# Optimization experiments

Hardware: AMD Instinct MI355X
Metric: run time of the kernel (lower is better)

Reference implementation:

```python
import jax, jax.numpy as jnp
import numpy as np

EPS = 1e-5

def _ln(x, w, b):
    m = jnp.mean(x, axis=-1, keepdims=True)
    var = jnp.mean((x - m) ** 2, axis=-1, keepdims=True)
    return (x - m) / jnp.sqrt(var + EPS) * w + b

def setup_inputs() -> dict:
    key = jax.random.key(0)
    ks = jax.random.split(key, 24)
    B, Hh, Ww, C = 8, 96, 96, 512
    L = Hh * Ww
    heads, Ck, Cv, hidden = 8, 512, 512, 2048
    s = 0.02
    d = {
        'x': jax.random.normal(ks[0], (B, L, C), jnp.float32),
        'v': jax.random.normal(ks[1], (B, L, C), jnp.float32),
        'H': Hh, 'W': Ww,
        'ln1_w': jnp.ones((C,), jnp.float32), 'ln1_b': jnp.zeros((C,), jnp.float32),
        'lnv_w': jnp.ones((C,), jnp.float32), 'lnv_b': jnp.zeros((C,), jnp.float32),
        'ln2_w': jnp.ones((C,), jnp.float32), 'ln2_b': jnp.zeros((C,), jnp.float32),
        'wq': jax.random.normal(ks[2], (Ck, C), jnp.float32) * s,
        'bq': jnp.zeros((Ck,), jnp.float32),
        'wk': jax.random.normal(ks[3], (Ck, C), jnp.float32) * s,
        'bk': jnp.zeros((Ck,), jnp.float32),
        'wv': jax.random.normal(ks[4], (Cv, C), jnp.float32) * s,
        'bv': jnp.zeros((Cv,), jnp.float32),
        'wr': jax.random.normal(ks[5], (C, Cv), jnp.float32) * s,
        'br': jnp.zeros((C,), jnp.float32),
        'fc1_w': jax.random.normal(ks[6], (hidden, C), jnp.float32) * s,
        'fc1_b': jnp.zeros((hidden,), jnp.float32),
        'fc2_w': jax.random.normal(ks[7], (C, hidden), jnp.float32) * s,
        'fc2_b': jnp.zeros((C,), jnp.float32),
    }
    return d

def reference(x, v, H, W, ln1_w, ln1_b, lnv_w, lnv_b, ln2_w, ln2_b,
              wq, bq, wk, bk, wv, bv, wr, br, fc1_w, fc1_b, fc2_w, fc2_b):
    B, L, C = x.shape
    heads = 8
    Ck, Cv = wq.shape[0], wv.shape[0]
    dk, dv = Ck // heads, Cv // heads

    shortcut = x
    xn = _ln(x, ln1_w, ln1_b)             # (B,L,C)
    vn = _ln(v, lnv_w, lnv_b)             # (B,L,C)

    # 1x1 convs == per-pixel linear over channels
    q = xn @ wq.T + bq                     # (B,L,Ck)
    k = vn @ wk.T + bk                     # (B,L,Ck)
    val = vn @ wv.T + bv                   # (B,L,Cv)

    q = q.reshape(B, L, heads, dk)
    k = k.reshape(B, L, heads, dk)
    val = val.reshape(B, L, heads, dv)

    k_sm = jax.nn.softmax(k, axis=1)       # softmax over spatial dim (torch dim=2 on (n,ck,hw))
    q_sm = jax.nn.softmax(q, axis=3)       # softmax over per-head key channels (torch dim=1)

    # context: (B, heads, dk, dv) = key @ value^T
    context = jnp.einsum('blhk,blhv->bhkv', k_sm, val)
    # attended: (B, heads, dv, L) = context^T @ query  (channel-major like torch)
    attended = jnp.einsum('bhkv,blhk->bhvl', context, q_sm)
    agg = attended.reshape(B, Cv, L)        # concat heads along channels

    reproj = jnp.einsum('oc,bcl->bol', wr, agg) + br[None, :, None]  # (B,C,L)
    x_bcl = jnp.transpose(xn, (0, 2, 1))    # residual inside attention (normed x, channel-major)
    attn_bcl = reproj + x_bcl               # (B,C,L) ~ torch (B,C,H,W) contiguous
    # faithful to torch .view(B, H*W, v_dim): raw row-major reinterpret, no transpose
    attn = attn_bcl.reshape(B, L, C)

    x1 = attn + shortcut
    h = _ln(x1, ln2_w, ln2_b)
    h = jax.nn.gelu(h @ fc1_w.T + fc1_b, approximate=False)
    h = h @ fc2_w.T + fc2_b
    out = x1 + h
    return out
```

## Files before the change

### kernel.cpp

```cpp
#include <hip/hip_runtime.h>
#include <math.h>

typedef unsigned short u16;
typedef unsigned int   u32;
typedef __bf16 bf16x8 __attribute__((ext_vector_type(8)));
typedef float  floatx4 __attribute__((ext_vector_type(4)));

#define DEVFN static __device__ __forceinline__

#define Bb   8
#define Ll   9216
#define Cc   512
#define BL   73728
#define HID  2048

DEVFN float bfu2f(u16 u) { union { u32 i; float f; } z; z.i = ((u32)u) << 16; return z.f; }
DEVFN u16 f2bfu(float f) {
    union { float f; u32 i; } z; z.f = f;
    u32 i = z.i;
    i += 0x7fffu + ((i >> 16) & 1u);
    return (u16)(i >> 16);
}

DEVFN void unpack8(uint4 v, float* x) {
    x[0] = bfu2f(v.x & 0xffff); x[1] = bfu2f(v.x >> 16);
    x[2] = bfu2f(v.y & 0xffff); x[3] = bfu2f(v.y >> 16);
    x[4] = bfu2f(v.z & 0xffff); x[5] = bfu2f(v.z >> 16);
    x[6] = bfu2f(v.w & 0xffff); x[7] = bfu2f(v.w >> 16);
}
DEVFN uint4 pack8(const float* x) {
    uint4 v;
    v.x = (u32)f2bfu(x[0]) | ((u32)f2bfu(x[1]) << 16);
    v.y = (u32)f2bfu(x[2]) | ((u32)f2bfu(x[3]) << 16);
    v.z = (u32)f2bfu(x[4]) | ((u32)f2bfu(x[5]) << 16);
    v.w = (u32)f2bfu(x[6]) | ((u32)f2bfu(x[7]) << 16);
    return v;
}

DEVFN void async16(const void* g, void* l) {
    __builtin_amdgcn_global_load_lds((const __attribute__((address_space(1))) void*)g,
                                     (__attribute__((address_space(3))) void*)l, 16, 0, 0);
}

__global__ __launch_bounds__(256) void f2b(const float* __restrict__ s, u16* __restrict__ d, int n) {
    const int i = blockIdx.x * 256 + threadIdx.x;
    if (i < n) d[i] = f2bfu(s[i]);
}

__global__ __launch_bounds__(256) void ln512(const float* __restrict__ in_,
                                             const float* __restrict__ w, const float* __restrict__ b,
                                             u16* __restrict__ out) {
    const int wave = threadIdx.x >> 6, lane = threadIdx.x & 63;
    const int row = blockIdx.x * 4 + wave;
    float x[8];
    const float4* p = (const float4*)(in_ + (size_t)row * 512);
    float4 a = p[lane * 2], c = p[lane * 2 + 1];
    x[0] = a.x; x[1] = a.y; x[2] = a.z; x[3] = a.w;
    x[4] = c.x; x[5] = c.y; x[6] = c.z; x[7] = c.w;
    float s = 0.f, s2 = 0.f;
    #pragma unroll
    for (int j = 0; j < 8; ++j) { s += x[j]; s2 += x[j] * x[j]; }
    #pragma unroll
    for (int off = 32; off >= 1; off >>= 1) { s += __shfl_xor(s, off); s2 += __shfl_xor(s2, off); }
    const float m   = s * (1.f / 512.f);
    const float var = s2 * (1.f / 512.f) - m * m;
    const float r   = rsqrtf(var + 1e-5f);
    float y[8];
    const int c0 = lane * 8;
    #pragma unroll
    for (int j = 0; j < 8; ++j)
        y[j] = (x[j] - m) * r * w[c0 + j] + b[c0 + j];
    ((uint4*)(out + (size_t)row * 512))[lane] = pack8(y);
}

template<int EPI>
__global__ __launch_bounds__(256) void gemm_bt(
    const u16* __restrict__ A, const u16* __restrict__ W, const float* __restrict__ bias,
    const float* __restrict__ resid, void* __restrict__ out_,
    int M, int N, int K, int wbatch) {
    __shared__ __align__(16) u16 sA[128 * 32];
    __shared__ __align__(16) u16 sB[128 * 32];
    const int t = threadIdx.x;
    const int wv = t >> 6, lane = t & 63;
    const int row0 = blockIdx.y * 128, col0 = blockIdx.x * 128;
    const u16* Wb = W + (wbatch > 0 ? (size_t)(row0 / wbatch) * (size_t)N * (size_t)K : 0);
    const int wr = wv >> 1, wc = wv & 1;
    floatx4 acc[4][4] = {};
    const int rr = t >> 2, kc = t & 3;
    const int mrow = lane & 15, koff = (lane >> 4) * 8;

    for (int k0 = 0; k0 < K; k0 += 32) {
        #pragma unroll
        for (int i = 0; i < 2; ++i) {
            const u16* ga = A  + (size_t)(row0 + i * 64 + rr) * K + (k0 + kc * 8);
            const u16* gb = Wb + (size_t)(col0 + i * 64 + rr) * K + (k0 + kc * 8);
            async16(ga, (char*)sA + (i * 256 + wv * 64) * 16);
            async16(gb, (char*)sB + (i * 256 + wv * 64) * 16);
        }
        __syncthreads();
        bf16x8 af[4], bq[4];
        #pragma unroll
        for (int mi = 0; mi < 4; ++mi)
            af[mi] = *(const bf16x8*)&sA[(wr * 64 + mi * 16 + mrow) * 32 + koff];
        #pragma unroll
        for (int ni = 0; ni < 4; ++ni)
            bq[ni] = *(const bf16x8*)&sB[(wc * 64 + ni * 16 + mrow) * 32 + koff];
        #pragma unroll
        for (int mi = 0; mi < 4; ++mi)
            #pragma unroll
            for (int ni = 0; ni < 4; ++ni)
                acc[mi][ni] = __builtin_amdgcn_mfma_f32_16x16x32_bf16(af[mi], bq[ni], acc[mi][ni], 0, 0, 0);
        __syncthreads();
    }
    #pragma unroll
    for (int mi = 0; mi < 4; ++mi) {
        #pragma unroll
        for (int ni = 0; ni < 4; ++ni) {
            const int col = col0 + wc * 64 + ni * 16 + mrow;
            const float bb = bias[col];
            #pragma unroll
            for (int r = 0; r < 4; ++r) {
                const int row = row0 + wr * 64 + mi * 16 + (lane >> 4) * 4 + r;
                float v2 = acc[mi][ni][r] + bb;
                if (EPI == 1) v2 = 0.5f * v2 * (1.f + erff(v2 * 0.70710678118654752f));
                if (EPI == 2) {
                    v2 += resid[(size_t)row * N + col];
                    ((float*)out_)[(size_t)row * N + col] = v2;
                } else {
                    ((u16*)out_)[(size_t)row * N + col] = f2bfu(v2);
                }
            }
        }
    }
}

__global__ __launch_bounds__(256) void kstats1(const u16* __restrict__ k,
                                               float* __restrict__ pmax, float* __restrict__ psum) {
    const int cg = blockIdx.x, lc = blockIdx.y, b = blockIdx.z;
    const int t = threadIdx.x, cl = t & 15, lsub = t >> 4;
    const int c = cg * 16 + cl;
    const u16* base = k + ((size_t)b * Ll + (size_t)lc * 1152) * 512 + c;
    float m = -1e30f, s = 0.f;
    for (int i = 0; i < 72; ++i) {
        const float x = bfu2f(base[(size_t)(lsub + i * 16) * 512]);
        const float nm = fmaxf(m, x);
        s = s * __expf(m - nm) + __expf(x - nm);
        m = nm;
    }
    __shared__ float sm[256], ss[256];
    sm[t] = m; ss[t] = s;
    __syncthreads();
    if (t < 16) {
        float M = sm[t], S = ss[t];
        for (int j = 1; j < 16; ++j) {
            const float m2 = sm[j * 16 + t], s2 = ss[j * 16 + t];
            const float nm = fmaxf(M, m2);
            S = S * __expf(M - nm) + s2 * __expf(m2 - nm);
            M = nm;
        }
        const int cid = b * 512 + cg * 16 + t;
        pmax[(size_t)cid * 8 + lc] = M;
        psum[(size_t)cid * 8 + lc] = S;
    }
}

__global__ __launch_bounds__(256) void kstats2(const float* __restrict__ pmax, const float* __restrict__ psum,
                                               float* __restrict__ kmax, float* __restrict__ ksum) {
    const int id = blockIdx.x * 256 + threadIdx.x;
    float M = -1e30f, S = 0.f;
    for (int lc = 0; lc < 8; ++lc) {
        const float m2 = pmax[(size_t)id * 8 + lc], s2 = psum[(size_t)id * 8 + lc];
        const float nm = fmaxf(M, m2);
        S = S * __expf(M - nm) + s2 * __expf(m2 - nm);
        M = nm;
    }
    kmax[id] = M; ksum[id] = S;
}

__global__ __launch_bounds__(256) void zerof(float* __restrict__ p) {
    p[blockIdx.x * 256 + threadIdx.x] = 0.f;
}

__global__ __launch_bounds__(256) void ctxk(const u16* __restrict__ k, const u16* __restrict__ val,
                                            const float* __restrict__ kmax, float* __restrict__ ctx) {
    const int lc = blockIdx.x, h = blockIdx.y, b = blockIdx.z;
    const int t = threadIdx.x;
    const int li = t >> 6, cc = t & 63;
    const int dkt = t >> 4, dvt = t & 15;
    __shared__ __align__(16) float ke[4][64];
    __shared__ __align__(16) float ve[4][64];
    float acc[4][4] = {};
    const size_t rowbase = ((size_t)b * Ll + (size_t)lc * 1152) * 512 + h * 64;
    const float km = kmax[b * 512 + h * 64 + cc];
    for (int l0 = 0; l0 < 1152; l0 += 4) {
        const float kf = bfu2f(k[rowbase + (size_t)(l0 + li) * 512 + cc]);
        const float vf = bfu2f(val[rowbase + (size_t)(l0 + li) * 512 + cc]);
        __syncthreads();
        ke[li][cc] = __expf(kf - km);
        ve[li][cc] = vf;
        __syncthreads();
        #pragma unroll
        for (int li2 = 0; li2 < 4; ++li2) {
            const float4 kk = *(const float4*)&ke[li2][dkt * 4];
            const float4 vv = *(const float4*)&ve[li2][dvt * 4];
            acc[0][0] += kk.x * vv.x; acc[0][1] += kk.x * vv.y; acc[0][2] += kk.x * vv.z; acc[0][3] += kk.x * vv.w;
            acc[1][0] += kk.y * vv.x; acc[1][1] += kk.y * vv.y; acc[1][2] += kk.y * vv.z; acc[1][3] += kk.y * vv.w;
            acc[2][0] += kk.z * vv.x; acc[2][1] += kk.z * vv.y; acc[2][2] += kk.z * vv.z; acc[2][3] += kk.z * vv.w;
            acc[3][0] += kk.w * vv.x; acc[3][1] += kk.w * vv.y; acc[3][2] += kk.w * vv.z; acc[3][3] += kk.w * vv.w;
        }
    }
    float* cp = ctx + (((size_t)(b * 8 + h) * 64 + dkt * 4) * 64 + dvt * 4);
    #pragma unroll
    for (int i = 0; i < 4; ++i)
        #pragma unroll
        for (int j = 0; j < 4; ++j)
            atomicAdd(&cp[(size_t)i * 64 + j], acc[i][j]);
}

__global__ __launch_bounds__(256) void qsm(u16* __restrict__ q) {
    const size_t seg = (size_t)blockIdx.x * 256 + threadIdx.x;
    u16* p = q + seg * 64;
    float x[64];
    #pragma unroll
    for (int i = 0; i < 8; ++i) { uint4 v = ((const uint4*)p)[i]; unpack8(v, x + i * 8); }
    float m = x[0];
    #pragma unroll
    for (int i = 1; i < 64; ++i) m = fmaxf(m, x[i]);
    float s = 0.f;
    #pragma unroll
    for (int i = 0; i < 64; ++i) { x[i] = __expf(x[i] - m); s += x[i]; }
    const float inv = 1.f / s;
    #pragma unroll
    for (int i = 0; i < 64; ++i) x[i] *= inv;
    #pragma unroll
    for (int i = 0; i < 8; ++i) ((uint4*)p)[i] = pack8(x + i * 8);
}

__global__ __launch_bounds__(256) void weffk(const float* __restrict__ ctx, const float* __restrict__ wr,
                                             const float* __restrict__ ksum, u16* __restrict__ weff) {
    const int b = blockIdx.y;
    const int idx = blockIdx.x * 256 + threadIdx.x;
    const int co = idx >> 9, ck = idx & 511;
    const int h = ck >> 6, dk = ck & 63;
    const float* wrp = wr + (size_t)co * 512 + h * 64;
    const float* cp = ctx + ((size_t)(b * 8 + h) * 64 + dk) * 64;
    float s = 0.f;
    #pragma unroll 8
    for (int dv = 0; dv < 64; ++dv) s += wrp[dv] * cp[dv];
    s /= ksum[b * 512 + ck];
    weff[((size_t)b * 512 + co) * 512 + ck] = f2bfu(s);
}

__global__ __launch_bounds__(256) void assemble(const u16* __restrict__ attnCT, const u16* __restrict__ xn,
                                                const float* __restrict__ x, float* __restrict__ x1) {
    const int ct = blockIdx.x, lt = blockIdx.y, b = blockIdx.z;
    __shared__ float tile[64][65];
    const int t = threadIdx.x, j = t & 63, i0 = t >> 6;
    const size_t base = ((size_t)b * Ll + (size_t)lt * 64) * 512 + ct * 64;
    #pragma unroll
    for (int ii = 0; ii < 16; ++ii) {
        const int i = i0 + ii * 4;
        tile[i][j] = bfu2f(attnCT[base + (size_t)i * 512 + j]) + bfu2f(xn[base + (size_t)i * 512 + j]);
    }
    __syncthreads();
    const size_t bb = (size_t)b * Ll * 512;
    #pragma unroll
    for (int ii = 0; ii < 16; ++ii) {
        const int co = i0 + ii * 4;
        const size_t n = (size_t)(ct * 64 + co) * Ll + (size_t)lt * 64 + j;
        x1[bb + n] = tile[j][co] + x[bb + n];
    }
}

extern "C" void kernel_launch(void* const* d_in, const int* in_sizes, int n_in,
                              void* d_out, int out_size, void* d_ws, size_t ws_size,
                              hipStream_t stream) {
    (void)in_sizes; (void)n_in; (void)out_size; (void)ws_size;
    const float* x    = (const float*)d_in[0];
    const float* v    = (const float*)d_in[1];
    const float* ln1w = (const float*)d_in[4];
    const float* ln1b = (const float*)d_in[5];
    const float* lnvw = (const float*)d_in[6];
    const float* lnvb = (const float*)d_in[7];
    const float* ln2w = (const float*)d_in[8];
    const float* ln2b = (const float*)d_in[9];
    const float* wq   = (const float*)d_in[10]; const float* bq_ = (const float*)d_in[11];
    const float* wk   = (const float*)d_in[12]; const float* bk_ = (const float*)d_in[13];
    const float* wv_  = (const float*)d_in[14]; const float* bv_ = (const float*)d_in[15];
    const float* wr_  = (const float*)d_in[16]; const float* br_ = (const float*)d_in[17];
    const float* f1w  = (const float*)d_in[18]; const float* f1b = (const float*)d_in[19];
    const float* f2w  = (const float*)d_in[20]; const float* f2b_ = (const float*)d_in[21];
    float* out = (float*)d_out;

    char* ws = (char*)d_ws;
    u16*   xn   = (u16*)(ws);
    u16*   vn   = (u16*)(ws + 75497472ull);
    u16*   q    = (u16*)(ws + 150994944ull);
    u16*   kk   = (u16*)(ws + 226492416ull);
    u16*   val  = (u16*)(ws + 301989888ull);
    float* x1   = (float*)(ws + 377487360ull);
    float* kmax = (float*)(ws + 528482304ull);
    float* ksum = (float*)(ws + 528498688ull);
    float* pmax = (float*)(ws + 528515072ull);
    float* psum = (float*)(ws + 528646144ull);
    float* ctx  = (float*)(ws + 528777216ull);
    u16*   weff = (u16*)(ws + 529825792ull);
    u16*   bwq  = (u16*)(ws + 534020096ull);
    u16*   bwk  = (u16*)(ws + 534544384ull);
    u16*   bwv  = (u16*)(ws + 535068672ull);
    u16*   bf1  = (u16*)(ws + 535592960ull);
    u16*   bf2  = (u16*)(ws + 537690112ull);

    f2b<<<1024, 256, 0, stream>>>(wq,  bwq, 262144);
    f2b<<<1024, 256, 0, stream>>>(wk,  bwk, 262144);
    f2b<<<1024, 256, 0, stream>>>(wv_, bwv, 262144);
    f2b<<<4096, 256, 0, stream>>>(f1w, bf1, 1048576);
    f2b<<<4096, 256, 0, stream>>>(f2w, bf2, 1048576);
    ln512<<<18432, 256, 0, stream>>>(x, ln1w, ln1b, xn);
    ln512<<<18432, 256, 0, stream>>>(v, lnvw, lnvb, vn);
    gemm_bt<0><<<dim3(4, 576), 256, 0, stream>>>(xn, bwq, bq_, nullptr, q,   BL, 512, 512, 0);
    gemm_bt<0><<<dim3(4, 576), 256, 0, stream>>>(vn, bwk, bk_, nullptr, kk,  BL, 512, 512, 0);
    gemm_bt<0><<<dim3(4, 576), 256, 0, stream>>>(vn, bwv, bv_, nullptr, val, BL, 512, 512, 0);
    kstats1<<<dim3(32, 8, 8), 256, 0, stream>>>(kk, pmax, psum);
    kstats2<<<16, 256, 0, stream>>>(pmax, psum, kmax, ksum);
    zerof<<<1024, 256, 0, stream>>>(ctx);
    ctxk<<<dim3(8, 8, 8), 256, 0, stream>>>(kk, val, kmax, ctx);
    qsm<<<2304, 256, 0, stream>>>(q);
    weffk<<<dim3(1024, 8), 256, 0, stream>>>(ctx, wr_, ksum, weff);
    gemm_bt<0><<<dim3(4, 576), 256, 0, stream>>>(q, weff, br_, nullptr, vn , BL, 512, 512, Ll);
    assemble<<<dim3(8, 144, 8), 256, 0, stream>>>(vn, xn, x, x1);
    ln512<<<18432, 256, 0, stream>>>(x1, ln2w, ln2b, q );
    for (int c2 = 0; c2 < 4; ++c2) {
        const size_t m0 = (size_t)c2 * 18432;
        gemm_bt<1><<<dim3(16, 144), 256, 0, stream>>>(q + m0 * 512, bf1, f1b, nullptr, kk,
                                                      18432, HID, 512, 0);
        gemm_bt<2><<<dim3(4, 144), 256, 0, stream>>>(kk, bf2, f2b_, x1 + m0 * 512, out + m0 * 512,
                                                     18432, 512, HID, 0);
    }
}
```

Measured before the change: 1.850 ms.

## Vectorize key-softmax stats and context kernels with wider row tiles and prefetch

kstats1 now has each thread load 8 bf16 channels with uint4 and software-prefetch the next row. The grid becomes 128 chunks by 8 batches, so there are more partials and kstats2 merges 128 of them. ctxk loads k and val with 16-byte vector loads, stages 32 rows per shared-memory tile instead of 4 (fewer barriers per row), prefetches the next tile, and doubles the number of L-chunks to raise parallelism. The partial-stat buffers are aliased onto the x1 region, which is not yet written at that point. The risks are more shared memory per block and more atomic traffic on ctx.

```diff
diff --git a/kernel.cpp b/kernel.cpp
--- a/kernel.cpp
+++ b/kernel.cpp
@@ -136,31 +136,42 @@
 
 __global__ __launch_bounds__(256) void kstats1(const u16* __restrict__ k,
                                                float* __restrict__ pmax, float* __restrict__ psum) {
-    const int cg = blockIdx.x, lc = blockIdx.y, b = blockIdx.z;
-    const int t = threadIdx.x, cl = t & 15, lsub = t >> 4;
-    const int c = cg * 16 + cl;
-    const u16* base = k + ((size_t)b * Ll + (size_t)lc * 1152) * 512 + c;
-    float m = -1e30f, s = 0.f;
-    for (int i = 0; i < 72; ++i) {
-        const float x = bfu2f(base[(size_t)(lsub + i * 16) * 512]);
-        const float nm = fmaxf(m, x);
-        s = s * __expf(m - nm) + __expf(x - nm);
-        m = nm;
-    }
-    __shared__ float sm[256], ss[256];
-    sm[t] = m; ss[t] = s;
+    const int lc = blockIdx.x, b = blockIdx.y;
+    const int t = threadIdx.x, c8 = t & 63, rg = t >> 6;
+    const u16* base = k + ((size_t)b * Ll + (size_t)lc * 72 + rg) * 512 + c8 * 8;
+    float m[8], s[8];
+    #pragma unroll
+    for (int j = 0; j < 8; ++j) { m[j] = -1e30f; s[j] = 0.f; }
+    uint4 v = *(const uint4*)base;
+    for (int i = 0; i < 18; ++i) {
+        uint4 vnxt;
+        if (i + 1 < 18) vnxt = *(const uint4*)&base[(size_t)(i + 1) * 4 * 512];
+        float x[8]; unpack8(v, x);
+        #pragma unroll
+        for (int j = 0; j < 8; ++j) {
+            const float nm = fmaxf(m[j], x[j]);
+            s[j] = s[j] * __expf(m[j] - nm) + __expf(x[j] - nm);
+            m[j] = nm;
+        }
+        v = vnxt;
+    }
+    __shared__ float sm[4][512], ss[4][512];
+    #pragma unroll
+    for (int j = 0; j < 8; ++j) { sm[rg][c8 * 8 + j] = m[j]; ss[rg][c8 * 8 + j] = s[j]; }
     __syncthreads();
-    if (t < 16) {
-        float M = sm[t], S = ss[t];
-        for (int j = 1; j < 16; ++j) {
-            const float m2 = sm[j * 16 + t], s2 = ss[j * 16 + t];
+    #pragma unroll
+    for (int cp = 0; cp < 2; ++cp) {
+        const int c = t + cp * 256;
+        float M = sm[0][c], S = ss[0][c];
+        #pragma unroll
+        for (int r = 1; r < 4; ++r) {
+            const float m2 = sm[r][c], s2 = ss[r][c];
             const float nm = fmaxf(M, m2);
             S = S * __expf(M - nm) + s2 * __expf(m2 - nm);
             M = nm;
         }
-        const int cid = b * 512 + cg * 16 + t;
-        pmax[(size_t)cid * 8 + lc] = M;
-        psum[(size_t)cid * 8 + lc] = S;
+        pmax[(size_t)lc * 4096 + b * 512 + c] = M;
+        psum[(size_t)lc * 4096 + b * 512 + c] = S;
     }
 }
 
@@ -168,8 +179,8 @@
                                                float* __restrict__ kmax, float* __restrict__ ksum) {
     const int id = blockIdx.x * 256 + threadIdx.x;
     float M = -1e30f, S = 0.f;
-    for (int lc = 0; lc < 8; ++lc) {
-        const float m2 = pmax[(size_t)id * 8 + lc], s2 = psum[(size_t)id * 8 + lc];
+    for (int lc = 0; lc < 128; ++lc) {
+        const float m2 = pmax[(size_t)lc * 4096 + id], s2 = psum[(size_t)lc * 4096 + id];
         const float nm = fmaxf(M, m2);
         S = S * __expf(M - nm) + s2 * __expf(m2 - nm);
         M = nm;
@@ -181,32 +192,45 @@
     p[blockIdx.x * 256 + threadIdx.x] = 0.f;
 }
 
-__global__ __launch_bounds__(256) void ctxk(const u16* __restrict__ k, const u16* __restrict__ val,
-                                            const float* __restrict__ kmax, float* __restrict__ ctx) {
+__global__ __launch_bounds__(256, 4) void ctxk(const u16* __restrict__ k, const u16* __restrict__ val,
+                                               const float* __restrict__ kmax, float* __restrict__ ctx) {
     const int lc = blockIdx.x, h = blockIdx.y, b = blockIdx.z;
     const int t = threadIdx.x;
-    const int li = t >> 6, cc = t & 63;
+    const int lrow = t >> 3, lcol = t & 7;
     const int dkt = t >> 4, dvt = t & 15;
-    __shared__ __align__(16) float ke[4][64];
-    __shared__ __align__(16) float ve[4][64];
+    __shared__ __align__(16) float ke[32][64];
+    __shared__ __align__(16) float ve[32][64];
     float acc[4][4] = {};
-    const size_t rowbase = ((size_t)b * Ll + (size_t)lc * 1152) * 512 + h * 64;
-    const float km = kmax[b * 512 + h * 64 + cc];
-    for (int l0 = 0; l0 < 1152; l0 += 4) {
-        const float kf = bfu2f(k[rowbase + (size_t)(l0 + li) * 512 + cc]);
-        const float vf = bfu2f(val[rowbase + (size_t)(l0 + li) * 512 + cc]);
+    const size_t rowbase = ((size_t)b * Ll + (size_t)lc * 576) * 512 + h * 64 + lcol * 8;
+    float km[8];
+    {
+        const float* kmb = kmax + b * 512 + h * 64 + lcol * 8;
+        #pragma unroll
+        for (int j = 0; j < 8; ++j) km[j] = kmb[j];
+    }
+    uint4 kv = *(const uint4*)&k[rowbase + (size_t)lrow * 512];
+    uint4 vv = *(const uint4*)&val[rowbase + (size_t)lrow * 512];
+    for (int l0 = 0; l0 < 576; l0 += 32) {
+        float kf[8], vf[8];
+        unpack8(kv, kf); unpack8(vv, vf);
         __syncthreads();
-        ke[li][cc] = __expf(kf - km);
-        ve[li][cc] = vf;
+        #pragma unroll
+        for (int j = 0; j < 8; ++j) ke[lrow][lcol * 8 + j] = __expf(kf[j] - km[j]);
+        #pragma unroll
+        for (int j = 0; j < 8; ++j) ve[lrow][lcol * 8 + j] = vf[j];
         __syncthreads();
-        #pragma unroll
-        for (int li2 = 0; li2 < 4; ++li2) {
+        if (l0 + 32 < 576) {
+            kv = *(const uint4*)&k[rowbase + (size_t)(l0 + 32 + lrow) * 512];
+            vv = *(const uint4*)&val[rowbase + (size_t)(l0 + 32 + lrow) * 512];
+        }
+        #pragma unroll
+        for (int li2 = 0; li2 < 32; ++li2) {
             const float4 kk = *(const float4*)&ke[li2][dkt * 4];
-            const float4 vv = *(const float4*)&ve[li2][dvt * 4];
-            acc[0][0] += kk.x * vv.x; acc[0][1] += kk.x * vv.y; acc[0][2] += kk.x * vv.z; acc[0][3] += kk.x * vv.w;
-            acc[1][0] += kk.y * vv.x; acc[1][1] += kk.y * vv.y; acc[1][2] += kk.y * vv.z; acc[1][3] += kk.y * vv.w;
-            acc[2][0] += kk.z * vv.x; acc[2][1] += kk.z * vv.y; acc[2][2] += kk.z * vv.z; acc[2][3] += kk.z * vv.w;
-            acc[3][0] += kk.w * vv.x; acc[3][1] += kk.w * vv.y; acc[3][2] += kk.w * vv.z; acc[3][3] += kk.w * vv.w;
+            const float4 vv2 = *(const float4*)&ve[li2][dvt * 4];
+            acc[0][0] += kk.x * vv2.x; acc[0][1] += kk.x * vv2.y; acc[0][2] += kk.x * vv2.z; acc[0][3] += kk.x * vv2.w;
+            acc[1][0] += kk.y * vv2.x; acc[1][1] += kk.y * vv2.y; acc[1][2] += kk.y * vv2.z; acc[1][3] += kk.y * vv2.w;
+            acc[2][0] += kk.z * vv2.x; acc[2][1] += kk.z * vv2.y; acc[2][2] += kk.z * vv2.z; acc[2][3] += kk.z * vv2.w;
+            acc[3][0] += kk.w * vv2.x; acc[3][1] += kk.w * vv2.y; acc[3][2] += kk.w * vv2.z; acc[3][3] += kk.w * vv2.w;
         }
     }
     float* cp = ctx + (((size_t)(b * 8 + h) * 64 + dkt * 4) * 64 + dvt * 4);
@@ -301,8 +325,6 @@
     float* x1   = (float*)(ws + 377487360ull);
     float* kmax = (float*)(ws + 528482304ull);
     float* ksum = (float*)(ws + 528498688ull);
-    float* pmax = (float*)(ws + 528515072ull);
-    float* psum = (float*)(ws + 528646144ull);
     float* ctx  = (float*)(ws + 528777216ull);
     u16*   weff = (u16*)(ws + 529825792ull);
     u16*   bwq  = (u16*)(ws + 534020096ull);
@@ -310,6 +332,8 @@
     u16*   bwv  = (u16*)(ws + 535068672ull);
     u16*   bf1  = (u16*)(ws + 535592960ull);
     u16*   bf2  = (u16*)(ws + 537690112ull);
+    float* pmax = x1;
+    float* psum = x1 + 524288;
 
     f2b<<<1024, 256, 0, stream>>>(wq,  bwq, 262144);
     f2b<<<1024, 256, 0, stream>>>(wk,  bwk, 262144);
@@ -321,10 +345,10 @@
     gemm_bt<0><<<dim3(4, 576), 256, 0, stream>>>(xn, bwq, bq_, nullptr, q,   BL, 512, 512, 0);
     gemm_bt<0><<<dim3(4, 576), 256, 0, stream>>>(vn, bwk, bk_, nullptr, kk,  BL, 512, 512, 0);
     gemm_bt<0><<<dim3(4, 576), 256, 0, stream>>>(vn, bwv, bv_, nullptr, val, BL, 512, 512, 0);
-    kstats1<<<dim3(32, 8, 8), 256, 0, stream>>>(kk, pmax, psum);
+    kstats1<<<dim3(128, 8), 256, 0, stream>>>(kk, pmax, psum);
     kstats2<<<16, 256, 0, stream>>>(pmax, psum, kmax, ksum);
     zerof<<<1024, 256, 0, stream>>>(ctx);
-    ctxk<<<dim3(8, 8, 8), 256, 0, stream>>>(kk, val, kmax, ctx);
+    ctxk<<<dim3(16, 8, 8), 256, 0, stream>>>(kk, val, kmax, ctx);
     qsm<<<2304, 256, 0, stream>>>(q);
     weffk<<<dim3(1024, 8), 256, 0, stream>>>(ctx, wr_, ksum, weff);
     gemm_bt<0><<<dim3(4, 576), 256, 0, stream>>>(q, weff, br_, nullptr, vn , BL, 512, 512, Ll);
```

Result: faster. 1.789 ms (-3.3%).
